# Kernel optimization log

Hardware: AMD Instinct MI355X
Metric: run time of the kernel (lower is better)

## Reference

```python
import jax, jax.numpy as jnp
import numpy as np

NUM_EXPERTS = 8
TOP_K = 2

def setup_inputs() -> dict:
    key = jax.random.key(0)
    ks = jax.random.split(key, 5)
    B, S, D, F, E = 4, 2048, 1024, 4096, NUM_EXPERTS
    x = jax.random.normal(ks[0], (B, S, D), dtype=jnp.float32)
    router_w = jax.random.normal(ks[1], (D, E), dtype=jnp.float32) * 0.02
    router_b = jnp.zeros((E,), dtype=jnp.float32)
    w1 = jax.random.normal(ks[2], (E, D, F), dtype=jnp.float32) * 0.02
    b1 = jnp.zeros((E, F), dtype=jnp.float32)
    w2 = jax.random.normal(ks[3], (E, F, D), dtype=jnp.float32) * 0.02
    b2 = jnp.zeros((E, D), dtype=jnp.float32)
    return {"x": x, "router_w": router_w, "router_b": router_b,
            "w1": w1, "b1": b1, "w2": w2, "b2": b2}

def reference(x, router_w, router_b, w1, b1, w2, b2):
    B, S, D = x.shape
    E = router_w.shape[1]
    x_flat = x.reshape(-1, D)                                  # [N, D]
    router_probs = jax.nn.softmax(x_flat @ router_w + router_b, axis=-1)  # [N, E]
    topk_probs, topk_idx = jax.lax.top_k(router_probs, TOP_K)  # [N, K]
    topk_probs = topk_probs / jnp.sum(topk_probs, axis=-1, keepdims=True)
    # combine weight per (token, expert): sum over top-k slots assigned to that expert
    cw = jnp.sum(topk_probs[..., None] * jax.nn.one_hot(topk_idx, E, dtype=x.dtype), axis=1)  # [N, E]
    out = jnp.zeros_like(x_flat)
    for e in range(E):  # small fixed expert count; each iter is a dense GEMM pair
        h = jax.nn.gelu(x_flat @ w1[e] + b1[e], approximate=False)  # [N, F]
        out = out + cw[:, e:e + 1] * (h @ w2[e] + b2[e])            # [N, D]
    return out.reshape(B, S, D)
```

## Files before the change

kernel.cpp:

```cpp
#include <hip/hip_runtime.h>
#include <hip/hip_bf16.h>

typedef __attribute__((ext_vector_type(8))) __bf16 bf16x8;
typedef __attribute__((ext_vector_type(4))) float f32x4;

#define NTOK 8192
#define D_DIM 1024
#define F_DIM 4096
#define NEXP 8
#define SLOT_TOT 16384
#define SLOT_CAP 16512

__device__ __forceinline__ unsigned short f2b(float f) {
  __hip_bfloat16 b = __float2bfloat16(f);
  return reinterpret_cast<unsigned short&>(b);
}

__device__ __forceinline__ void gload_lds16(const void* g, void* l) {
  __builtin_amdgcn_global_load_lds(
      (__attribute__((address_space(1))) void*)g,
      (__attribute__((address_space(3))) void*)l, 16, 0, 0);
}


__global__ void init_counts_kernel(int* counts) {
  if (threadIdx.x < NEXP) counts[threadIdx.x] = 0;
}

__global__ void zero_out_kernel(float* out) {
  const int i = blockIdx.x * 256 + threadIdx.x;
  reinterpret_cast<float4*>(out)[i] = make_float4(0.f, 0.f, 0.f, 0.f);
}

__global__ void convert_x_kernel(const float* __restrict__ x,
                                 __hip_bfloat16* __restrict__ xb) {
  const int i = (blockIdx.x * 256 + threadIdx.x) * 4;
  const float4 v = *reinterpret_cast<const float4*>(x + i);
  union { unsigned short u[4]; uint2 d; } o;
  o.u[0] = f2b(v.x); o.u[1] = f2b(v.y); o.u[2] = f2b(v.z); o.u[3] = f2b(v.w);
  *reinterpret_cast<uint2*>(xb + i) = o.d;
}

__global__ void transpose_conv_kernel(const float* __restrict__ src,
                                      __hip_bfloat16* __restrict__ dst,
                                      int R, int C) {
  __shared__ float tile[64][65];
  const int e = blockIdx.z;
  src += (size_t)e * R * C;
  dst += (size_t)e * R * C;
  const int c0 = blockIdx.x * 64, r0 = blockIdx.y * 64;
  const int tx = threadIdx.x, ty = threadIdx.y;
  #pragma unroll
  for (int j = 0; j < 4; ++j) {
    const float4 v = *reinterpret_cast<const float4*>(
        &src[(size_t)(r0 + ty + j * 16) * C + c0 + tx * 4]);
    tile[ty + j * 16][tx * 4 + 0] = v.x;
    tile[ty + j * 16][tx * 4 + 1] = v.y;
    tile[ty + j * 16][tx * 4 + 2] = v.z;
    tile[ty + j * 16][tx * 4 + 3] = v.w;
  }
  __syncthreads();
  #pragma unroll
  for (int j = 0; j < 4; ++j) {
    const int c = ty + j * 16;
    union { unsigned short u[4]; uint2 d; } o;
    #pragma unroll
    for (int i = 0; i < 4; ++i) o.u[i] = f2b(tile[tx * 4 + i][c]);
    *reinterpret_cast<uint2*>(&dst[(size_t)(c0 + c) * R + r0 + tx * 4]) = o.d;
  }
}

__global__ void router_kernel(const float* __restrict__ x,
                              const float* __restrict__ rw,
                              const float* __restrict__ rb,
                              int* __restrict__ topk_idx,
                              float* __restrict__ topk_w,
                              int* __restrict__ counts) {
  __shared__ float rwT[NEXP * D_DIM];
  const int tid = threadIdx.x;
  for (int i = tid; i < NEXP * D_DIM; i += 256) {
    const int d = i >> 3, e = i & 7;
    rwT[e * D_DIM + d] = rw[i];
  }
  __syncthreads();

  const int wave = tid >> 6, lane = tid & 63;
  const int tok = blockIdx.x * 4 + wave;
  const float* xr = x + (size_t)tok * D_DIM;

  float acc[NEXP];
  #pragma unroll
  for (int e = 0; e < NEXP; ++e) acc[e] = 0.f;

  for (int i = 0; i < D_DIM / 64; ++i) {
    const int d = i * 64 + lane;
    const float xv = xr[d];
    #pragma unroll
    for (int e = 0; e < NEXP; ++e) acc[e] += xv * rwT[e * D_DIM + d];
  }
  #pragma unroll
  for (int off = 32; off > 0; off >>= 1) {
    #pragma unroll
    for (int e = 0; e < NEXP; ++e) acc[e] += __shfl_xor(acc[e], off);
  }

  if (lane == 0) {
    float l[NEXP];
    #pragma unroll
    for (int e = 0; e < NEXP; ++e) l[e] = acc[e] + rb[e];
    int i1 = 0;
    #pragma unroll
    for (int e = 1; e < NEXP; ++e) if (l[e] > l[i1]) i1 = e;
    int i2 = (i1 == 0) ? 1 : 0;
    #pragma unroll
    for (int e = 0; e < NEXP; ++e) if (e != i1 && e != i2 && l[e] > l[i2]) i2 = e;
    const float w1 = 1.f / (1.f + __expf(l[i2] - l[i1]));
    topk_idx[tok * 2 + 0] = i1;
    topk_idx[tok * 2 + 1] = i2;
    topk_w[tok * 2 + 0] = w1;
    topk_w[tok * 2 + 1] = 1.f - w1;
    atomicAdd(&counts[i1], 1);
    atomicAdd(&counts[i2], 1);
  }
}

__global__ void offsets_kernel(const int* __restrict__ counts,
                               int* __restrict__ offsets,
                               int* __restrict__ cursors,
                               int* __restrict__ slot_token,
                               float* __restrict__ slot_cw) {
  const int t = threadIdx.x;
  if (t == 0) {
    int s = 0;
    for (int e = 0; e < NEXP; ++e) { offsets[e] = s; cursors[e] = s; s += counts[e]; }
    offsets[NEXP] = s;
  }
  if (t < SLOT_CAP - SLOT_TOT) {
    slot_token[SLOT_TOT + t] = 0;
    slot_cw[SLOT_TOT + t] = 0.f;
  }
}

__global__ void scatter_kernel(const int* __restrict__ topk_idx,
                               const float* __restrict__ topk_w,
                               int* __restrict__ cursors,
                               int* __restrict__ slot_token,
                               float* __restrict__ slot_cw) {
  const int tok = blockIdx.x * 256 + threadIdx.x;
  if (tok >= NTOK) return;
  #pragma unroll
  for (int k = 0; k < 2; ++k) {
    const int e = topk_idx[tok * 2 + k];
    const int p = atomicAdd(&cursors[e], 1);
    slot_token[p] = tok;
    slot_cw[p] = topk_w[tok * 2 + k];
  }
}

template <int PHASE>
__global__ __launch_bounds__(256, 4) void moe_gemm(
    const __hip_bfloat16* __restrict__ A,
    const __hip_bfloat16* __restrict__ B,
    const float* __restrict__ bias,
    const int* __restrict__ slot_token,
    const float* __restrict__ slot_cw,
    const int* __restrict__ counts,
    const int* __restrict__ offsets,
    __hip_bfloat16* __restrict__ Hout,
    float* __restrict__ Out) {
  constexpr int K = (PHASE == 1) ? D_DIM : F_DIM;
  constexpr int NCOL = (PHASE == 1) ? F_DIM : D_DIM;
  constexpr int KT = K / 32;

  const int e = blockIdx.z;
  const int cnt = counts[e];
  const int mt = blockIdx.y;
  if (mt * 128 >= cnt) return;
  const int nt = blockIdx.x;
  const int base = offsets[e];

  __shared__ unsigned short lA[2][4096];
  __shared__ unsigned short lB[2][4096];

  const int tid = threadIdx.x;
  const int w = tid >> 6, lane = tid & 63;
  const int r = lane & 15, kg = lane >> 4;
  const int wm = w >> 1, wn = w & 1;

  const int rowA0 = mt * 128 + w * 16 + r;
  const int rowA1 = mt * 128 + (4 + w) * 16 + r;
  const __hip_bfloat16 *gA0, *gA1;
  if constexpr (PHASE == 1) {
    gA0 = A + (size_t)slot_token[base + rowA0] * K + kg * 8;
    gA1 = A + (size_t)slot_token[base + rowA1] * K + kg * 8;
  } else {
    gA0 = A + (size_t)(base + rowA0) * K + kg * 8;
    gA1 = A + (size_t)(base + rowA1) * K + kg * 8;
  }
  const __hip_bfloat16* Be = B + (size_t)e * NCOL * K;
  const __hip_bfloat16* gB0 = Be + (size_t)(nt * 128 + w * 16 + r) * K + kg * 8;
  const __hip_bfloat16* gB1 = Be + (size_t)(nt * 128 + (4 + w) * 16 + r) * K + kg * 8;

  f32x4 acc[4][4] = {};

#define STAGE(b) do {                       \
    gload_lds16(gA0, &lA[b][w * 512]);      \
    gload_lds16(gA1, &lA[b][(4 + w) * 512]);\
    gload_lds16(gB0, &lB[b][w * 512]);      \
    gload_lds16(gB1, &lB[b][(4 + w) * 512]);\
    gA0 += 32; gA1 += 32; gB0 += 32; gB1 += 32; } while (0)

#define COMPUTE(b) do {                                                     \
    bf16x8 af[4], bfr[4];                                                   \
    _Pragma("unroll") for (int i = 0; i < 4; ++i) {                         \
      af[i]  = *(const bf16x8*)&lA[b][(wm * 4 + i) * 512 + lane * 8];       \
      bfr[i] = *(const bf16x8*)&lB[b][(wn * 4 + i) * 512 + lane * 8];       \
    }                                                                       \
    _Pragma("unroll") for (int mi = 0; mi < 4; ++mi)                        \
      _Pragma("unroll") for (int ni = 0; ni < 4; ++ni)                      \
        acc[mi][ni] = __builtin_amdgcn_mfma_f32_16x16x32_bf16(             \
            af[mi], bfr[ni], acc[mi][ni], 0, 0, 0); } while (0)

  STAGE(0);
  __syncthreads();
  int cur = 0;
  for (int kt = 0; kt < KT - 1; ++kt) {
    STAGE(cur ^ 1);
    COMPUTE(cur);
    __syncthreads();
    cur ^= 1;
  }
  COMPUTE(cur);

#undef STAGE
#undef COMPUTE

  const int rem = cnt - mt * 128;
  const int q4 = (lane >> 4) * 4;

  if constexpr (PHASE == 1) {
    #pragma unroll
    for (int ni = 0; ni < 4; ++ni) {
      const int col = nt * 128 + wn * 64 + ni * 16 + (lane & 15);
      const float bv = bias[e * NCOL + col];
      #pragma unroll
      for (int mi = 0; mi < 4; ++mi) {
        #pragma unroll
        for (int rr = 0; rr < 4; ++rr) {
          const int rloc = wm * 64 + mi * 16 + q4 + rr;
          if (rloc < rem) {
            float v = acc[mi][ni][rr] + bv;
            v = 0.5f * v * (1.f + erff(v * 0.70710678118654752f));
            Hout[(size_t)(base + mt * 128 + rloc) * F_DIM + col] = __float2bfloat16(v);
          }
        }
      }
    }
  } else {
    #pragma unroll
    for (int mi = 0; mi < 4; ++mi) {
      int toks[4]; float cws[4];
      #pragma unroll
      for (int rr = 0; rr < 4; ++rr) {
        const int rloc = wm * 64 + mi * 16 + q4 + rr;
        const int slot = base + mt * 128 + rloc;
        const bool ok = (rloc < rem);
        toks[rr] = ok ? slot_token[slot] : -1;
        cws[rr]  = ok ? slot_cw[slot] : 0.f;
      }
      #pragma unroll
      for (int ni = 0; ni < 4; ++ni) {
        const int col = nt * 128 + wn * 64 + ni * 16 + (lane & 15);
        const float bv = bias[e * NCOL + col];
        #pragma unroll
        for (int rr = 0; rr < 4; ++rr) {
          if (toks[rr] >= 0)
            atomicAdd(&Out[(size_t)toks[rr] * D_DIM + col], cws[rr] * (acc[mi][ni][rr] + bv));
        }
      }
    }
  }
}


extern "C" void kernel_launch(void* const* d_in, const int* in_sizes, int n_in,
                              void* d_out, int out_size, void* d_ws, size_t ws_size,
                              hipStream_t stream) {
  const float* x  = (const float*)d_in[0];
  const float* rw = (const float*)d_in[1];
  const float* rb = (const float*)d_in[2];
  const float* w1 = (const float*)d_in[3];
  const float* b1 = (const float*)d_in[4];
  const float* w2 = (const float*)d_in[5];
  const float* b2 = (const float*)d_in[6];
  float* out = (float*)d_out;

  char* p = (char*)d_ws;
  size_t used = 0;
  auto carve = [&](size_t bytes) {
    char* r = p + used;
    used += (bytes + 255) & ~(size_t)255;
    return (void*)r;
  };
  __hip_bfloat16* xb  = (__hip_bfloat16*)carve((size_t)NTOK * D_DIM * 2);
  __hip_bfloat16* w1t = (__hip_bfloat16*)carve((size_t)NEXP * F_DIM * D_DIM * 2);
  __hip_bfloat16* w2t = (__hip_bfloat16*)carve((size_t)NEXP * D_DIM * F_DIM * 2);
  __hip_bfloat16* h   = (__hip_bfloat16*)carve((size_t)SLOT_CAP * F_DIM * 2);
  int*   topk_idx   = (int*)carve((size_t)NTOK * 2 * 4);
  float* topk_w     = (float*)carve((size_t)NTOK * 2 * 4);
  int*   slot_token = (int*)carve((size_t)SLOT_CAP * 4);
  float* slot_cw    = (float*)carve((size_t)SLOT_CAP * 4);
  int* counts  = (int*)carve(256);
  int* offsets = (int*)carve(256);
  int* cursors = (int*)carve(256);

  zero_out_kernel<<<8192, 256, 0, stream>>>(out);
  if (used > ws_size) return;

  init_counts_kernel<<<1, 64, 0, stream>>>(counts);
  router_kernel<<<NTOK / 4, 256, 0, stream>>>(x, rw, rb, topk_idx, topk_w, counts);
  offsets_kernel<<<1, 256, 0, stream>>>(counts, offsets, cursors, slot_token, slot_cw);
  scatter_kernel<<<NTOK / 256, 256, 0, stream>>>(topk_idx, topk_w, cursors, slot_token, slot_cw);

  convert_x_kernel<<<(NTOK * D_DIM) / (256 * 4), 256, 0, stream>>>(x, xb);
  dim3 tb(16, 16);
  transpose_conv_kernel<<<dim3(F_DIM / 64, D_DIM / 64, NEXP), tb, 0, stream>>>(w1, w1t, D_DIM, F_DIM);
  transpose_conv_kernel<<<dim3(D_DIM / 64, F_DIM / 64, NEXP), tb, 0, stream>>>(w2, w2t, F_DIM, D_DIM);

  moe_gemm<1><<<dim3(F_DIM / 128, 64, NEXP), 256, 0, stream>>>(
      xb, w1t, b1, slot_token, slot_cw, counts, offsets, h, nullptr);
  moe_gemm<2><<<dim3(D_DIM / 128, 64, NEXP), 256, 0, stream>>>(
      h, w2t, b2, slot_token, slot_cw, counts, offsets, nullptr, out);
}
```

Baseline: 1.106 ms.

## Use 256x128 tiles with 512 threads and a triple-buffered LDS pipeline

```diff
diff --git a/kernel.cpp b/kernel.cpp
--- a/kernel.cpp
+++ b/kernel.cpp
@@ -9,7 +9,7 @@
 #define F_DIM 4096
 #define NEXP 8
 #define SLOT_TOT 16384
-#define SLOT_CAP 16512
+#define SLOT_CAP 16640
 
 __device__ __forceinline__ unsigned short f2b(float f) {
   __hip_bfloat16 b = __float2bfloat16(f);
@@ -158,7 +158,7 @@
 }
 
 template <int PHASE>
-__global__ __launch_bounds__(256, 4) void moe_gemm(
+__global__ __launch_bounds__(512, 4) void moe_gemm(
     const __hip_bfloat16* __restrict__ A,
     const __hip_bfloat16* __restrict__ B,
     const float* __restrict__ bias,
@@ -175,20 +175,20 @@
   const int e = blockIdx.z;
   const int cnt = counts[e];
   const int mt = blockIdx.y;
-  if (mt * 128 >= cnt) return;
+  if (mt * 256 >= cnt) return;
   const int nt = blockIdx.x;
   const int base = offsets[e];
 
-  __shared__ unsigned short lA[2][4096];
-  __shared__ unsigned short lB[2][4096];
+  __shared__ unsigned short lA[3][8192];
+  __shared__ unsigned short lB[3][4096];
 
   const int tid = threadIdx.x;
   const int w = tid >> 6, lane = tid & 63;
   const int r = lane & 15, kg = lane >> 4;
   const int wm = w >> 1, wn = w & 1;
 
-  const int rowA0 = mt * 128 + w * 16 + r;
-  const int rowA1 = mt * 128 + (4 + w) * 16 + r;
+  const int rowA0 = mt * 256 + w * 16 + r;
+  const int rowA1 = mt * 256 + (w + 8) * 16 + r;
   const __hip_bfloat16 *gA0, *gA1;
   if constexpr (PHASE == 1) {
     gA0 = A + (size_t)slot_token[base + rowA0] * K + kg * 8;
@@ -199,43 +199,67 @@
   }
   const __hip_bfloat16* Be = B + (size_t)e * NCOL * K;
   const __hip_bfloat16* gB0 = Be + (size_t)(nt * 128 + w * 16 + r) * K + kg * 8;
-  const __hip_bfloat16* gB1 = Be + (size_t)(nt * 128 + (4 + w) * 16 + r) * K + kg * 8;
 
   f32x4 acc[4][4] = {};
 
-#define STAGE(b) do {                       \
-    gload_lds16(gA0, &lA[b][w * 512]);      \
-    gload_lds16(gA1, &lA[b][(4 + w) * 512]);\
-    gload_lds16(gB0, &lB[b][w * 512]);      \
-    gload_lds16(gB1, &lB[b][(4 + w) * 512]);\
-    gA0 += 32; gA1 += 32; gB0 += 32; gB1 += 32; } while (0)
-
-#define COMPUTE(b) do {                                                     \
-    bf16x8 af[4], bfr[4];                                                   \
-    _Pragma("unroll") for (int i = 0; i < 4; ++i) {                         \
-      af[i]  = *(const bf16x8*)&lA[b][(wm * 4 + i) * 512 + lane * 8];       \
-      bfr[i] = *(const bf16x8*)&lB[b][(wn * 4 + i) * 512 + lane * 8];       \
-    }                                                                       \
-    _Pragma("unroll") for (int mi = 0; mi < 4; ++mi)                        \
-      _Pragma("unroll") for (int ni = 0; ni < 4; ++ni)                      \
-        acc[mi][ni] = __builtin_amdgcn_mfma_f32_16x16x32_bf16(             \
-            af[mi], bfr[ni], acc[mi][ni], 0, 0, 0); } while (0)
-
-  STAGE(0);
-  __syncthreads();
-  int cur = 0;
-  for (int kt = 0; kt < KT - 1; ++kt) {
-    STAGE(cur ^ 1);
-    COMPUTE(cur);
-    __syncthreads();
-    cur ^= 1;
-  }
-  COMPUTE(cur);
-
-#undef STAGE
-#undef COMPUTE
-
-  const int rem = cnt - mt * 128;
+  auto stage = [&](unsigned short* pa, unsigned short* pb) {
+    gload_lds16(gA0, pa + w * 512);
+    gload_lds16(gA1, pa + (w + 8) * 512);
+    gload_lds16(gB0, pb + w * 512);
+    gA0 += 32; gA1 += 32; gB0 += 32;
+  };
+  auto compute = [&](const unsigned short* pa, const unsigned short* pb) {
+    bf16x8 af[4], bfr[4];
+    #pragma unroll
+    for (int i = 0; i < 4; ++i) {
+      af[i]  = *(const bf16x8*)(pa + (wm * 4 + i) * 512 + lane * 8);
+      bfr[i] = *(const bf16x8*)(pb + (wn * 4 + i) * 512 + lane * 8);
+    }
+    #pragma unroll
+    for (int mi = 0; mi < 4; ++mi)
+      #pragma unroll
+      for (int ni = 0; ni < 4; ++ni)
+        acc[mi][ni] = __builtin_amdgcn_mfma_f32_16x16x32_bf16(
+            af[mi], bfr[ni], acc[mi][ni], 0, 0, 0);
+  };
+
+  unsigned short *pa0 = lA[0], *pa1 = lA[1], *pa2 = lA[2];
+  unsigned short *pb0 = lB[0], *pb1 = lB[1], *pb2 = lB[2];
+
+  stage(pa0, pb0);
+  stage(pa1, pb1);
+  stage(pa2, pb2);
+
+  for (int t = 0; t < KT - 3; ++t) {
+    asm volatile("s_waitcnt vmcnt(6)" ::: "memory");
+    __builtin_amdgcn_sched_barrier(0);
+    __builtin_amdgcn_s_barrier();
+    __builtin_amdgcn_sched_barrier(0);
+    compute(pa0, pb0);
+    __builtin_amdgcn_sched_barrier(0);
+    __builtin_amdgcn_s_barrier();
+    __builtin_amdgcn_sched_barrier(0);
+    stage(pa0, pb0);
+    unsigned short* ta = pa0; pa0 = pa1; pa1 = pa2; pa2 = ta;
+    unsigned short* tb = pb0; pb0 = pb1; pb1 = pb2; pb2 = tb;
+  }
+  asm volatile("s_waitcnt vmcnt(6)" ::: "memory");
+  __builtin_amdgcn_sched_barrier(0);
+  __builtin_amdgcn_s_barrier();
+  __builtin_amdgcn_sched_barrier(0);
+  compute(pa0, pb0);
+  asm volatile("s_waitcnt vmcnt(3)" ::: "memory");
+  __builtin_amdgcn_sched_barrier(0);
+  __builtin_amdgcn_s_barrier();
+  __builtin_amdgcn_sched_barrier(0);
+  compute(pa1, pb1);
+  asm volatile("s_waitcnt vmcnt(0)" ::: "memory");
+  __builtin_amdgcn_sched_barrier(0);
+  __builtin_amdgcn_s_barrier();
+  __builtin_amdgcn_sched_barrier(0);
+  compute(pa2, pb2);
+
+  const int rem = cnt - mt * 256;
   const int q4 = (lane >> 4) * 4;
 
   if constexpr (PHASE == 1) {
@@ -251,7 +275,7 @@
           if (rloc < rem) {
             float v = acc[mi][ni][rr] + bv;
             v = 0.5f * v * (1.f + erff(v * 0.70710678118654752f));
-            Hout[(size_t)(base + mt * 128 + rloc) * F_DIM + col] = __float2bfloat16(v);
+            Hout[(size_t)(base + mt * 256 + rloc) * F_DIM + col] = __float2bfloat16(v);
           }
         }
       }
@@ -263,7 +287,7 @@
       #pragma unroll
       for (int rr = 0; rr < 4; ++rr) {
         const int rloc = wm * 64 + mi * 16 + q4 + rr;
-        const int slot = base + mt * 128 + rloc;
+        const int slot = base + mt * 256 + rloc;
         const bool ok = (rloc < rem);
         toks[rr] = ok ? slot_token[slot] : -1;
         cws[rr]  = ok ? slot_cw[slot] : 0.f;
@@ -327,8 +351,8 @@
   transpose_conv_kernel<<<dim3(F_DIM / 64, D_DIM / 64, NEXP), tb, 0, stream>>>(w1, w1t, D_DIM, F_DIM);
   transpose_conv_kernel<<<dim3(D_DIM / 64, F_DIM / 64, NEXP), tb, 0, stream>>>(w2, w2t, F_DIM, D_DIM);
 
-  moe_gemm<1><<<dim3(F_DIM / 128, 64, NEXP), 256, 0, stream>>>(
+  moe_gemm<1><<<dim3(F_DIM / 128, 32, NEXP), 512, 0, stream>>>(
       xb, w1t, b1, slot_token, slot_cw, counts, offsets, h, nullptr);
-  moe_gemm<2><<<dim3(D_DIM / 128, 64, NEXP), 256, 0, stream>>>(
+  moe_gemm<2><<<dim3(D_DIM / 128, 32, NEXP), 512, 0, stream>>>(
       h, w2t, b2, slot_token, slot_cw, counts, offsets, nullptr, out);
 }
```

Result: faster. 1.070 ms (-3.3%).
